# Optimization experiments

Hardware: AMD Instinct MI355X
Metric: run time of the kernel (lower is better)

## Reference

```python
import jax, jax.numpy as jnp
import numpy as np

B, T, LD, PD, W, NL = 2048, 256, 32, 8, 64, 3
TH, CH = LD * 2, W * 2  # token/channel mixing hidden dims (expansion=2)


def setup_inputs() -> dict:
    key = jax.random.key(0)
    ks = jax.random.split(key, 12)
    n = lambda k, s, sc=0.02: jax.random.normal(k, s, jnp.float32) * sc
    return {
        "phys": jax.random.normal(ks[0], (B, T, PD), jnp.float32),
        "latents": jax.random.uniform(ks[1], (B, LD), jnp.float32),
        "pos_emb": n(ks[2], (1, LD, W)),
        "tokW": n(ks[3], (1, W)), "tokb": jnp.zeros((W,), jnp.float32),
        "physW1": n(ks[4], (PD, W)), "physb1": jnp.zeros((W,), jnp.float32),
        "physW2": n(ks[5], (W, W)), "physb2": jnp.zeros((W,), jnp.float32),
        "tn_g": jnp.ones((NL, W), jnp.float32), "tn_b": jnp.zeros((NL, W), jnp.float32),
        "tiW": n(ks[6], (NL, LD, TH)), "tib": jnp.zeros((NL, TH), jnp.float32),
        "toW": n(ks[7], (NL, TH, LD)), "tob": jnp.zeros((NL, LD), jnp.float32),
        "cn_g": jnp.ones((NL, W), jnp.float32), "cn_b": jnp.zeros((NL, W), jnp.float32),
        "ciW": n(ks[8], (NL, W, CH)), "cib": jnp.zeros((NL, CH), jnp.float32),
        "coW": n(ks[9], (NL, CH, W)), "cob": jnp.zeros((NL, W), jnp.float32),
        "hn_g": jnp.ones((W,), jnp.float32), "hn_b": jnp.zeros((W,), jnp.float32),
        "headW": n(ks[10], (W, 1), 0.0002),  # 0.02 init * 0.01 scaling from torch
        "headb": jnp.zeros((1,), jnp.float32),
    }


def _ln(x, g, b):
    m = jnp.mean(x, -1, keepdims=True)
    v = jnp.mean((x - m) ** 2, -1, keepdims=True)
    return (x - m) * jax.lax.rsqrt(v + 1e-5) * g + b


def reference(phys, latents, pos_emb, tokW, tokb, physW1, physb1, physW2, physb2,
              tn_g, tn_b, tiW, tib, toW, tob, cn_g, cn_b, ciW, cib, coW, cob,
              hn_g, hn_b, headW, headb):
    gelu = lambda x: jax.nn.gelu(x, approximate=False)  # torch nn.GELU default (exact)

    def step(current, phys_t):
        # token_projection of current[..., None]: Linear(1, W)
        tokens = current[:, :, None] * tokW[0] + tokb  # [B, LD, W]
        p = gelu(phys_t @ physW1 + physb1) @ physW2 + physb2  # [B, W]
        tokens = tokens + p[:, None, :] + pos_emb
        for i in range(NL):
            # token mixing: LN over width, mix across latent tokens
            mt = jnp.swapaxes(_ln(tokens, tn_g[i], tn_b[i]), 1, 2)  # [B, W, LD]
            mt = gelu(mt @ tiW[i] + tib[i]) @ toW[i] + tob[i]       # [B, W, LD]
            tokens = tokens + jnp.swapaxes(mt, 1, 2)
            # channel mixing over width
            mc = _ln(tokens, cn_g[i], cn_b[i])
            tokens = tokens + (gelu(mc @ ciW[i] + cib[i]) @ coW[i] + cob[i])
        delta = (_ln(tokens, hn_g, hn_b) @ headW + headb)[..., 0]  # [B, LD]
        new = jnp.clip(current + delta, 0.0, 1.0)
        return new, new

    _, outs = jax.lax.scan(step, latents, jnp.swapaxes(phys, 0, 1))  # [T, B, LD]
    return jnp.swapaxes(outs, 0, 1)  # [B, T, LD]
```

## Files before the change

### kernel.cpp

```cpp
#include <hip/hip_runtime.h>
#include <math.h>


namespace {
constexpr int Tt = 256, NL = 3;

typedef float    f32x4 __attribute__((ext_vector_type(4)));
typedef _Float16 half2 __attribute__((ext_vector_type(2)));
typedef _Float16 h16x4 __attribute__((ext_vector_type(4)));
typedef _Float16 h16x8 __attribute__((ext_vector_type(8)));

#define MFMA16(a, b, c) __builtin_amdgcn_mfma_f32_16x16x32_f16((a), (b), (c), 0, 0, 0)

__device__ __forceinline__ half2 h2c(float v) { return (half2)((_Float16)v); }
__device__ __forceinline__ half2 pkrtz(float a, float b) {
    return __builtin_bit_cast(half2, __builtin_amdgcn_cvt_pkrtz(a, b));
}
__device__ __forceinline__ void st4h(short* p, half2 a, half2 b) {
    uint2 v;
    v.x = __builtin_bit_cast(unsigned int, a);
    v.y = __builtin_bit_cast(unsigned int, b);
    *(uint2*)p = v;
}
__device__ __forceinline__ half2 gelu_pk(half2 x) {
    half2 tc = __builtin_elementwise_min(__builtin_elementwise_max(x, h2c(-3.0f)), h2c(3.0f));
    half2 s = (tc * tc) * h2c(0.125f);
    half2 p = s * h2c(0.1455169f) + h2c(-0.446340f);
    p = s * p + h2c(0.604927f);
    p = s * p + h2c(-0.529702f);
    p = s * p + h2c(0.3989423f);
    return x * (h2c(0.5f) + tc * p);
}
__device__ __forceinline__ float gelu_f(float x) {
    float tc = fminf(fmaxf(x, -3.f), 3.f);
    float s = tc * tc;
    float p = fmaf(s, 3.55266e-5f, -8.71758e-4f);
    p = fmaf(s, p, 9.45198e-3f);
    p = fmaf(s, p, -6.62128e-2f);
    p = fmaf(s, p, 0.3989423f);
    return x * fmaf(tc, p, 0.5f);
}
__device__ __forceinline__ float rowsum16(float x) {
    x += __builtin_bit_cast(float, __builtin_amdgcn_update_dpp(0, __builtin_bit_cast(int, x), 0x121, 0xf, 0xf, false));
    x += __builtin_bit_cast(float, __builtin_amdgcn_update_dpp(0, __builtin_bit_cast(int, x), 0x122, 0xf, 0xf, false));
    x += __builtin_bit_cast(float, __builtin_amdgcn_update_dpp(0, __builtin_bit_cast(int, x), 0x124, 0xf, 0xf, false));
    x += __builtin_bit_cast(float, __builtin_amdgcn_update_dpp(0, __builtin_bit_cast(int, x), 0x128, 0xf, 0xf, false));
    return x;
}

__device__ __forceinline__ short f2h(float x) {
    return __builtin_bit_cast(short, (_Float16)x);
}

__global__ void lno_prep(const float* __restrict__ tiW, const float* __restrict__ toW,
                         const float* __restrict__ ciW, const float* __restrict__ coW,
                         const float* __restrict__ physW2, short* __restrict__ wsf) {
    int id = blockIdx.x * 256 + threadIdx.x;
    if (id < 6144) {
        int j = id & 7, lane = (id >> 3) & 63, g = id >> 9;
        int il = g >> 2, u = g & 3;
        int m = u * 16 + (lane & 15), k = (lane >> 4) * 8 + j;
        wsf[id] = f2h(tiW[il * 2048 + k * 64 + m]);
    } else if (id < 12288) {
        int t = id - 6144;
        int j = t & 7, lane = (t >> 3) & 63, g = t >> 9;
        int il = g >> 2, mt2 = (g >> 1) & 1, ks = g & 1;
        int m = mt2 * 16 + (lane & 15), k = ks * 32 + (lane >> 4) * 8 + j;
        wsf[id] = f2h(toW[il * 2048 + k * 32 + m]);
    } else if (id < 36864) {
        int t = id - 12288;
        int j = t & 7, lane = (t >> 3) & 63, g = t >> 9;
        int il = g >> 4, mtc = (g >> 1) & 7, ks = g & 1;
        int m = mtc * 16 + (lane & 15), k = ks * 32 + (lane >> 4) * 8 + j;
        wsf[id] = f2h(ciW[il * 8192 + k * 128 + m]);
    } else if (id < 61440) {
        int t = id - 36864;
        int j = t & 7, lane = (t >> 3) & 63, g = t >> 9;
        int il = g >> 4, nt = (g >> 2) & 3, ks = g & 3;
        int n = nt * 16 + (lane & 15), k = ks * 32 + (lane >> 4) * 8 + j;
        wsf[id] = f2h(coW[il * 8192 + k * 64 + n]);
    } else if (id < 65536) {
        int t = id - 61440;
        int w = t >> 6, k = t & 63;
        ((float*)(wsf + 61440))[t] = physW2[k * 64 + w];
    }
}

__global__ void lno_phys(const float* __restrict__ phys, const float* __restrict__ physW1,
                         const float* __restrict__ physb1, const float* __restrict__ physW2,
                         const float* __restrict__ physb2, short* __restrict__ pout) {
    __shared__ float hsh[4][64];
    const int lane = threadIdx.x & 63, wv = threadIdx.x >> 6;
    const size_t bt = (size_t)blockIdx.x * 4 + wv;
    const float* pt = phys + bt * 8;
    float4 px0 = *(const float4*)pt, px1 = *(const float4*)(pt + 4);
    float a = physb1[lane];
    a = fmaf(px0.x, physW1[0 * 64 + lane], a);
    a = fmaf(px0.y, physW1[1 * 64 + lane], a);
    a = fmaf(px0.z, physW1[2 * 64 + lane], a);
    a = fmaf(px0.w, physW1[3 * 64 + lane], a);
    a = fmaf(px1.x, physW1[4 * 64 + lane], a);
    a = fmaf(px1.y, physW1[5 * 64 + lane], a);
    a = fmaf(px1.z, physW1[6 * 64 + lane], a);
    a = fmaf(px1.w, physW1[7 * 64 + lane], a);
    hsh[wv][lane] = gelu_f(a);
    float acc = physb2[lane];
#pragma unroll
    for (int k = 0; k < 64; ++k) acc = fmaf(hsh[wv][k], physW2[k * 64 + lane], acc);
    pout[bt * 64 + (lane & 15) * 4 + (lane >> 4)] = f2h(acc);
}

__global__ __launch_bounds__(128, 4) void lno_scan(
    const float* __restrict__ latents, const float* __restrict__ pos_emb,
    const float* __restrict__ tokW,    const float* __restrict__ tokb,
    const float* __restrict__ tn_g,    const float* __restrict__ tn_b,
    const float* __restrict__ tib,     const float* __restrict__ tob,
    const float* __restrict__ cn_g,    const float* __restrict__ cn_b,
    const float* __restrict__ cib,     const float* __restrict__ cob,
    const float* __restrict__ hn_g,    const float* __restrict__ hn_b,
    const float* __restrict__ headW,   const float* __restrict__ headb,
    const short* __restrict__ wsf,     const short* pbuf, float* out)
{
    __shared__ __align__(16) short yB[2048];
    __shared__ __align__(16) short hB[4096];
    __shared__ __align__(16) short scr[2][1024];

    const short* tiWF = wsf;
    const short* toWF = wsf + 6144;
    const short* ciWF = wsf + 12288;
    const short* coWF = wsf + 36864;

    const int tid = threadIdx.x, lane = tid & 63, sb = tid >> 6;
    const int q = lane >> 4, c = lane & 15;
    const int b = blockIdx.x;
    short* sc = scr[sb];

    float tokw_r[4], tokb_r[4], gh_r[4];
#pragma unroll
    for (int nt = 0; nt < 4; ++nt) {
        tokw_r[nt] = tokW[nt * 16 + c];
        tokb_r[nt] = tokb[nt * 16 + c];
        gh_r[nt]   = hn_g[nt * 16 + c] * headW[nt * 16 + c];
    }
    float bhp = 0.f;
#pragma unroll
    for (int nt = 0; nt < 4; ++nt) bhp = fmaf(hn_b[nt * 16 + c], headW[nt * 16 + c], bhp);
    const float bh = rowsum16(bhp) + headb[0];

    float pe_r[4][4];
#pragma unroll
    for (int nt = 0; nt < 4; ++nt)
#pragma unroll
        for (int r = 0; r < 4; ++r)
            pe_r[nt][r] = pos_emb[(sb * 16 + q * 4 + r) * 64 + nt * 16 + c];

    f32x4 cur = *(const f32x4*)(latents + b * 32 + sb * 16 + q * 4);
    f32x4 tok[4];

    auto stats = [&](f32x4& mean, f32x4& rsig) {
#pragma unroll
        for (int r = 0; r < 4; ++r) {
            float s = (tok[0][r] + tok[1][r]) + (tok[2][r] + tok[3][r]);
            float qq = tok[0][r] * tok[0][r];
            qq = fmaf(tok[1][r], tok[1][r], qq);
            qq = fmaf(tok[2][r], tok[2][r], qq);
            qq = fmaf(tok[3][r], tok[3][r], qq);
            s = rowsum16(s); qq = rowsum16(qq);
            float m = s * 0.015625f;
            float v = fmaf(-m, m, qq * 0.015625f);
            mean[r] = m;
            rsig[r] = __builtin_amdgcn_rsqf(v + 1e-5f);
        }
    };

#pragma unroll 1
    for (int t = 0; t < Tt; ++t) {
        const h16x4 pv = *(const h16x4*)(pbuf + ((size_t)b * Tt + t) * 64 + c * 4);
#pragma unroll
        for (int nt = 0; nt < 4; ++nt) {
            const float basep = tokb_r[nt] + (float)pv[nt];
#pragma unroll
            for (int r = 0; r < 4; ++r)
                tok[nt][r] = fmaf(cur[r], tokw_r[nt], basep + pe_r[nt][r]);
        }

#pragma unroll 1
        for (int il = 0; il < NL; ++il) {
            f32x4 mean, rsig;
            stats(mean, rsig);
#pragma unroll
            for (int nt = 0; nt < 4; ++nt) {
                const float tng = tn_g[il * 64 + nt * 16 + c];
                const float tnb = tn_b[il * 64 + nt * 16 + c];
                float y0 = fmaf((tok[nt][0] - mean[0]) * rsig[0], tng, tnb);
                float y1 = fmaf((tok[nt][1] - mean[1]) * rsig[1], tng, tnb);
                float y2 = fmaf((tok[nt][2] - mean[2]) * rsig[2], tng, tnb);
                float y3 = fmaf((tok[nt][3] - mean[3]) * rsig[3], tng, tnb);
                st4h(&yB[(nt * 64 + (sb * 2 + (q >> 1)) * 16 + c) * 8 + (q & 1) * 4],
                     pkrtz(y0, y1), pkrtz(y2, y3));
            }
            __syncthreads();
            h16x8 yfrag[4];
#pragma unroll
            for (int nt = 0; nt < 4; ++nt) yfrag[nt] = *(const h16x8*)&yB[(nt * 64 + lane) * 8];

#pragma unroll
            for (int uu = 0; uu < 2; ++uu) {
                const int u = sb * 2 + uu;
                const h16x8 a1 = *(const h16x8*)(tiWF + ((il * 4 + u) * 64 + lane) * 8);
                const f32x4 bi = *(const f32x4*)(tib + il * 64 + u * 16 + q * 4);
#pragma unroll
                for (int nt = 0; nt < 4; ++nt) {
                    f32x4 acc = MFMA16(a1, yfrag[nt], bi);
                    st4h(&hB[sb * 2048 + (nt * 64 + (uu * 2 + (q >> 1)) * 16 + c) * 8 + (q & 1) * 4],
                         gelu_pk(pkrtz(acc[0], acc[1])), gelu_pk(pkrtz(acc[2], acc[3])));
                }
            }
            {
                const f32x4 tb = *(const f32x4*)(tob + il * 32 + sb * 16 + q * 4);
#pragma unroll
                for (int nt = 0; nt < 4; ++nt) tok[nt] += tb;
            }
            __syncthreads();
#pragma unroll
            for (int h = 0; h < 2; ++h) {
                const h16x8 a2 = *(const h16x8*)(toWF + ((il * 4 + sb * 2 + h) * 64 + lane) * 8);
                h16x8 hf[4];
#pragma unroll
                for (int nt = 0; nt < 4; ++nt)
                    hf[nt] = *(const h16x8*)&hB[h * 2048 + (nt * 64 + lane) * 8];
#pragma unroll
                for (int nt = 0; nt < 4; ++nt) tok[nt] = MFMA16(a2, hf[nt], tok[nt]);
            }

            stats(mean, rsig);
#pragma unroll
            for (int nt = 0; nt < 4; ++nt) {
                const float cng = cn_g[il * 64 + nt * 16 + c];
                const float cnb = cn_b[il * 64 + nt * 16 + c];
#pragma unroll
                for (int r = 0; r < 4; ++r) {
                    float v = fmaf((tok[nt][r] - mean[r]) * rsig[r], cng, cnb);
                    sc[(nt >> 1) * 512 + (q * 2 + (c >> 3) + 16 * r + 8 * (nt & 1)) * 8 + (c & 7)] = f2h(v);
                }
            }
            h16x8 b3[2];
            {
                const int lp = ((c >> 2) * 2 + (q & 1)) + 8 * ((c & 3) * 2 + (q >> 1));
#pragma unroll
                for (int ks = 0; ks < 2; ++ks) b3[ks] = *(const h16x8*)&sc[ks * 512 + lp * 8];
            }
#pragma unroll
            for (int nt = 0; nt < 4; ++nt) {
                const float cv = cob[il * 64 + nt * 16 + c];
                tok[nt] += cv;
            }
#pragma unroll
            for (int hh = 0; hh < 2; ++hh) {
#pragma unroll
                for (int mm = 0; mm < 4; ++mm) {
                    const int mtc = hh * 4 + mm;
                    const h16x8 a30 = *(const h16x8*)(ciWF + il * 8192 + (mtc * 2 + 0) * 512 + lane * 8);
                    const h16x8 a31 = *(const h16x8*)(ciWF + il * 8192 + (mtc * 2 + 1) * 512 + lane * 8);
                    const f32x4 bi3 = *(const f32x4*)(cib + il * 128 + mtc * 16 + q * 4);
                    f32x4 acc = MFMA16(a30, b3[0], bi3);
                    acc = MFMA16(a31, b3[1], acc);
                    st4h(&sc[(((mtc >> 1) & 1) * 64 + ((mtc & 1) * 2 + (q >> 1)) * 16 + c) * 8 + (q & 1) * 4],
                         gelu_pk(pkrtz(acc[0], acc[1])), gelu_pk(pkrtz(acc[2], acc[3])));
                }
                h16x8 a4[2];
#pragma unroll
                for (int kk = 0; kk < 2; ++kk) a4[kk] = *(const h16x8*)&sc[(kk * 64 + lane) * 8];
#pragma unroll
                for (int nt = 0; nt < 4; ++nt) {
                    const h16x8 b40 = *(const h16x8*)(coWF + il * 8192 + (nt * 4 + hh * 2 + 0) * 512 + lane * 8);
                    const h16x8 b41 = *(const h16x8*)(coWF + il * 8192 + (nt * 4 + hh * 2 + 1) * 512 + lane * 8);
                    tok[nt] = MFMA16(a4[0], b40, tok[nt]);
                    tok[nt] = MFMA16(a4[1], b41, tok[nt]);
                }
            }
        }

        {
            f32x4 mean, rsig;
            stats(mean, rsig);
#pragma unroll
            for (int r = 0; r < 4; ++r) {
                float l = (tok[0][r] - mean[r]) * gh_r[0];
                l = fmaf(tok[1][r] - mean[r], gh_r[1], l);
                l = fmaf(tok[2][r] - mean[r], gh_r[2], l);
                l = fmaf(tok[3][r] - mean[r], gh_r[3], l);
                l = rowsum16(l);
                float nv = cur[r] + fmaf(rsig[r], l, bh);
                cur[r] = fminf(fmaxf(nv, 0.f), 1.f);
            }
            if (c == 0)
                *(f32x4*)(out + ((size_t)b * Tt + t) * 32 + sb * 16 + q * 4) = cur;
        }
    }
}
}

extern "C" void kernel_launch(void* const* d_in, const int* in_sizes, int n_in,
                              void* d_out, int out_size, void* d_ws, size_t ws_size,
                              hipStream_t stream) {
    (void)in_sizes; (void)n_in; (void)ws_size; (void)out_size;
    const float* phys    = (const float*)d_in[0];
    const float* latents = (const float*)d_in[1];
    const float* pos_emb = (const float*)d_in[2];
    const float* tokW    = (const float*)d_in[3];
    const float* tokb    = (const float*)d_in[4];
    const float* physW1  = (const float*)d_in[5];
    const float* physb1  = (const float*)d_in[6];
    const float* physW2  = (const float*)d_in[7];
    const float* physb2  = (const float*)d_in[8];
    const float* tn_g    = (const float*)d_in[9];
    const float* tn_b    = (const float*)d_in[10];
    const float* tiW     = (const float*)d_in[11];
    const float* tib     = (const float*)d_in[12];
    const float* toW     = (const float*)d_in[13];
    const float* tob     = (const float*)d_in[14];
    const float* cn_g    = (const float*)d_in[15];
    const float* cn_b    = (const float*)d_in[16];
    const float* ciW     = (const float*)d_in[17];
    const float* cib     = (const float*)d_in[18];
    const float* coW     = (const float*)d_in[19];
    const float* cob     = (const float*)d_in[20];
    const float* hn_g    = (const float*)d_in[21];
    const float* hn_b    = (const float*)d_in[22];
    const float* headW   = (const float*)d_in[23];
    const float* headb   = (const float*)d_in[24];

    lno_prep<<<dim3(256), dim3(256), 0, stream>>>(tiW, toW, ciW, coW, physW2, (short*)d_ws);
    lno_phys<<<dim3(131072), dim3(256), 0, stream>>>(phys, physW1, physb1, physW2, physb2,
                                                     (short*)d_out);
    lno_scan<<<dim3(2048), dim3(128), 0, stream>>>(
        latents, pos_emb, tokW, tokb, tn_g, tn_b, tib, tob,
        cn_g, cn_b, cib, cob, hn_g, hn_b, headW, headb,
        (const short*)d_ws, (const short*)d_out, (float*)d_out);
}
```

Baseline: 7.556 ms.

## Pack eight batch rows per block with LDS-resident weights and flag-based wave pairing

The scan kernel now runs 8 batch elements per 1024-thread block, with each pair of waves handling one element. All mixing weights and biases are staged once per block into LDS through global_load_lds, so they are no longer read from global memory on every step. The two __syncthreads per layer are replaced by per-pair release/acquire flag spin-waits, and the token-mixing GEMMs use 16x16x16 MFMA with fragments kept in registers to cut LDS round trips. The phys projection is also prefetched one step ahead. In exchange, the kernel uses about 140KB of LDS, which likely limits it to one block per CU and may reduce the latency hiding it had before.

```diff
diff --git a/kernel.cpp b/kernel.cpp
--- a/kernel.cpp
+++ b/kernel.cpp
@@ -10,9 +10,13 @@
 typedef _Float16 h16x4 __attribute__((ext_vector_type(4)));
 typedef _Float16 h16x8 __attribute__((ext_vector_type(8)));
 
-#define MFMA16(a, b, c) __builtin_amdgcn_mfma_f32_16x16x32_f16((a), (b), (c), 0, 0, 0)
+#define MFMA32(a, b, c) __builtin_amdgcn_mfma_f32_16x16x32_f16((a), (b), (c), 0, 0, 0)
+#define MFMA16(a, b, c) __builtin_amdgcn_mfma_f32_16x16x16f16((a), (b), (c), 0, 0, 0)
+#define REL(p, v) __hip_atomic_store((p), (v), __ATOMIC_RELEASE, __HIP_MEMORY_SCOPE_WORKGROUP)
+#define ACQ(p) __hip_atomic_load((p), __ATOMIC_ACQUIRE, __HIP_MEMORY_SCOPE_WORKGROUP)
 
 __device__ __forceinline__ half2 h2c(float v) { return (half2)((_Float16)v); }
+__device__ __forceinline__ f32x4 f4s(float v) { return (f32x4)v; }
 __device__ __forceinline__ half2 pkrtz(float a, float b) {
     return __builtin_bit_cast(half2, __builtin_amdgcn_cvt_pkrtz(a, b));
 }
@@ -22,6 +26,11 @@
     v.y = __builtin_bit_cast(unsigned int, b);
     *(uint2*)p = v;
 }
+__device__ __forceinline__ h16x4 h4(half2 a, half2 b) {
+    h16x4 v; v[0] = a[0]; v[1] = a[1]; v[2] = b[0]; v[3] = b[1]; return v;
+}
+__device__ __forceinline__ half2 lo2(h16x4 v) { half2 r; r[0] = v[0]; r[1] = v[1]; return r; }
+__device__ __forceinline__ half2 hi2(h16x4 v) { half2 r; r[0] = v[2]; r[1] = v[3]; return r; }
 __device__ __forceinline__ half2 gelu_pk(half2 x) {
     half2 tc = __builtin_elementwise_min(__builtin_elementwise_max(x, h2c(-3.0f)), h2c(3.0f));
     half2 s = (tc * tc) * h2c(0.125f);
@@ -47,7 +56,6 @@
     x += __builtin_bit_cast(float, __builtin_amdgcn_update_dpp(0, __builtin_bit_cast(int, x), 0x128, 0xf, 0xf, false));
     return x;
 }
-
 __device__ __forceinline__ short f2h(float x) {
     return __builtin_bit_cast(short, (_Float16)x);
 }
@@ -57,16 +65,18 @@
                          const float* __restrict__ physW2, short* __restrict__ wsf) {
     int id = blockIdx.x * 256 + threadIdx.x;
     if (id < 6144) {
-        int j = id & 7, lane = (id >> 3) & 63, g = id >> 9;
-        int il = g >> 2, u = g & 3;
-        int m = u * 16 + (lane & 15), k = (lane >> 4) * 8 + j;
-        wsf[id] = f2h(tiW[il * 2048 + k * 64 + m]);
+        int e = id & 255, tile = id >> 8;
+        int lane = e >> 2, j = e & 3;
+        int q = lane >> 4, cc = lane & 15;
+        int kc = tile & 1, u = (tile >> 1) & 3, il = tile >> 3;
+        wsf[id] = f2h(tiW[il * 2048 + (16 * kc + 4 * q + j) * 64 + 16 * u + cc]);
     } else if (id < 12288) {
         int t = id - 6144;
-        int j = t & 7, lane = (t >> 3) & 63, g = t >> 9;
-        int il = g >> 2, mt2 = (g >> 1) & 1, ks = g & 1;
-        int m = mt2 * 16 + (lane & 15), k = ks * 32 + (lane >> 4) * 8 + j;
-        wsf[id] = f2h(toW[il * 2048 + k * 32 + m]);
+        int e = t & 255, tile = t >> 8;
+        int lane = e >> 2, j = e & 3;
+        int q = lane >> 4, cc = lane & 15;
+        int kc = tile & 3, sb = (tile >> 2) & 1, il = tile >> 3;
+        wsf[id] = f2h(toW[il * 2048 + (16 * kc + 4 * q + j) * 32 + 16 * sb + cc]);
     } else if (id < 36864) {
         int t = id - 12288;
         int j = t & 7, lane = (t >> 3) & 63, g = t >> 9;
@@ -110,7 +120,7 @@
     pout[bt * 64 + (lane & 15) * 4 + (lane >> 4)] = f2h(acc);
 }
 
-__global__ __launch_bounds__(128, 4) void lno_scan(
+__global__ __launch_bounds__(1024, 4) void lno_scan(
     const float* __restrict__ latents, const float* __restrict__ pos_emb,
     const float* __restrict__ tokW,    const float* __restrict__ tokb,
     const float* __restrict__ tn_g,    const float* __restrict__ tn_b,
@@ -121,19 +131,44 @@
     const float* __restrict__ headW,   const float* __restrict__ headb,
     const short* __restrict__ wsf,     const short* pbuf, float* out)
 {
-    __shared__ __align__(16) short yB[2048];
-    __shared__ __align__(16) short hB[4096];
-    __shared__ __align__(16) short scr[2][1024];
-
-    const short* tiWF = wsf;
-    const short* toWF = wsf + 6144;
-    const short* ciWF = wsf + 12288;
-    const short* coWF = wsf + 36864;
-
-    const int tid = threadIdx.x, lane = tid & 63, sb = tid >> 6;
+    __shared__ __align__(16) short wAll[61440];
+    __shared__ __align__(16) short tbuf[8][2048];
+    __shared__ __align__(16) float biasL[1632];
+    __shared__ int flags[8][8];
+
+    const int tid = threadIdx.x, lane = tid & 63, wv = tid >> 6;
+    const int sb = wv & 1, tm = wv >> 1, pn = sb ^ 1;
     const int q = lane >> 4, c = lane & 15;
-    const int b = blockIdx.x;
-    short* sc = scr[sb];
+    const int b = blockIdx.x * 8 + tm;
+    short* buf = tbuf[tm];
+    short* mysc = buf + sb * 1024;
+    int* F = flags[tm];
+
+    const short* A1L = wAll;
+    const short* A2L = wAll + 6144;
+    const short* A3L = wAll + 12288;
+    const short* B4L = wAll + 36864;
+
+    if (wv < 15) {
+        const unsigned int* src = (const unsigned int*)wsf;
+#pragma unroll
+        for (int i = 0; i < 8; ++i) {
+            const int cid = wv * 8 + i;
+            __builtin_amdgcn_global_load_lds(src + cid * 256 + lane * 4,
+                                             (unsigned int*)&wAll[cid * 512], 16, 0, 0);
+        }
+    }
+    for (int i = tid; i < 192; i += 1024) {
+        biasL[i] = tib[i];
+        biasL[672 + i]  = tn_g[i];
+        biasL[864 + i]  = tn_b[i];
+        biasL[1056 + i] = cn_g[i];
+        biasL[1248 + i] = cn_b[i];
+        biasL[1440 + i] = cob[i];
+    }
+    for (int i = tid; i < 96;  i += 1024) biasL[192 + i] = tob[i];
+    for (int i = tid; i < 384; i += 1024) biasL[288 + i] = cib[i];
+    if (tid < 64) ((int*)flags)[tid] = 0;
 
     float tokw_r[4], tokb_r[4], gh_r[4];
 #pragma unroll
@@ -147,136 +182,192 @@
     for (int nt = 0; nt < 4; ++nt) bhp = fmaf(hn_b[nt * 16 + c], headW[nt * 16 + c], bhp);
     const float bh = rowsum16(bhp) + headb[0];
 
-    float pe_r[4][4];
+    f32x4 pe4[4];
 #pragma unroll
     for (int nt = 0; nt < 4; ++nt)
 #pragma unroll
         for (int r = 0; r < 4; ++r)
-            pe_r[nt][r] = pos_emb[(sb * 16 + q * 4 + r) * 64 + nt * 16 + c];
+            pe4[nt][r] = pos_emb[(sb * 16 + q * 4 + r) * 64 + nt * 16 + c];
 
     f32x4 cur = *(const f32x4*)(latents + b * 32 + sb * 16 + q * 4);
     f32x4 tok[4];
 
+    __syncthreads();
+
     auto stats = [&](f32x4& mean, f32x4& rsig) {
+        f32x4 s4 = (tok[0] + tok[1]) + (tok[2] + tok[3]);
+        f32x4 q4 = tok[0] * tok[0];
+        q4 = __builtin_elementwise_fma(tok[1], tok[1], q4);
+        q4 = __builtin_elementwise_fma(tok[2], tok[2], q4);
+        q4 = __builtin_elementwise_fma(tok[3], tok[3], q4);
 #pragma unroll
         for (int r = 0; r < 4; ++r) {
-            float s = (tok[0][r] + tok[1][r]) + (tok[2][r] + tok[3][r]);
-            float qq = tok[0][r] * tok[0][r];
-            qq = fmaf(tok[1][r], tok[1][r], qq);
-            qq = fmaf(tok[2][r], tok[2][r], qq);
-            qq = fmaf(tok[3][r], tok[3][r], qq);
-            s = rowsum16(s); qq = rowsum16(qq);
-            float m = s * 0.015625f;
+            float ss = rowsum16(s4[r]);
+            float qq = rowsum16(q4[r]);
+            float m = ss * 0.015625f;
             float v = fmaf(-m, m, qq * 0.015625f);
             mean[r] = m;
             rsig[r] = __builtin_amdgcn_rsqf(v + 1e-5f);
         }
     };
 
+    const short* pb = pbuf + (size_t)b * Tt * 64 + c * 4;
+    h16x4 pvc = *(const h16x4*)pb;
+
 #pragma unroll 1
     for (int t = 0; t < Tt; ++t) {
-        const h16x4 pv = *(const h16x4*)(pbuf + ((size_t)b * Tt + t) * 64 + c * 4);
+        const h16x4 pv = pvc;
+        if (t + 1 < Tt) pvc = *(const h16x4*)(pb + (t + 1) * 64);
+
 #pragma unroll
         for (int nt = 0; nt < 4; ++nt) {
-            const float basep = tokb_r[nt] + (float)pv[nt];
-#pragma unroll
-            for (int r = 0; r < 4; ++r)
-                tok[nt][r] = fmaf(cur[r], tokw_r[nt], basep + pe_r[nt][r]);
+            const f32x4 bp = f4s(tokb_r[nt] + (float)pv[nt]);
+            tok[nt] = __builtin_elementwise_fma(cur, f4s(tokw_r[nt]), pe4[nt] + bp);
         }
 
 #pragma unroll 1
         for (int il = 0; il < NL; ++il) {
+            const int g = t * 3 + il + 1;
             f32x4 mean, rsig;
             stats(mean, rsig);
+            h16x4 b1own[4];
 #pragma unroll
             for (int nt = 0; nt < 4; ++nt) {
-                const float tng = tn_g[il * 64 + nt * 16 + c];
-                const float tnb = tn_b[il * 64 + nt * 16 + c];
-                float y0 = fmaf((tok[nt][0] - mean[0]) * rsig[0], tng, tnb);
-                float y1 = fmaf((tok[nt][1] - mean[1]) * rsig[1], tng, tnb);
-                float y2 = fmaf((tok[nt][2] - mean[2]) * rsig[2], tng, tnb);
-                float y3 = fmaf((tok[nt][3] - mean[3]) * rsig[3], tng, tnb);
-                st4h(&yB[(nt * 64 + (sb * 2 + (q >> 1)) * 16 + c) * 8 + (q & 1) * 4],
-                     pkrtz(y0, y1), pkrtz(y2, y3));
-            }
-            __syncthreads();
-            h16x8 yfrag[4];
-#pragma unroll
-            for (int nt = 0; nt < 4; ++nt) yfrag[nt] = *(const h16x8*)&yB[(nt * 64 + lane) * 8];
-
+                const float tng = biasL[672 + il * 64 + nt * 16 + c];
+                const float tnb = biasL[864 + il * 64 + nt * 16 + c];
+                f32x4 y = __builtin_elementwise_fma((tok[nt] - mean) * rsig,
+                                                    f4s(tng), f4s(tnb));
+                half2 d0 = pkrtz(y[0], y[1]), d1 = pkrtz(y[2], y[3]);
+                b1own[nt] = h4(d0, d1);
+                st4h(&buf[sb * 1024 + (nt * 64 + lane) * 4], d0, d1);
+            }
+            if (lane == 0) REL(&F[sb], g);
+            {
+                const f32x4 tb = *(const f32x4*)&biasL[192 + il * 32 + sb * 16 + q * 4];
+#pragma unroll
+                for (int nt = 0; nt < 4; ++nt) tok[nt] += tb;
+            }
+            f32x4 hacc[2][4];
 #pragma unroll
             for (int uu = 0; uu < 2; ++uu) {
-                const int u = sb * 2 + uu;
-                const h16x8 a1 = *(const h16x8*)(tiWF + ((il * 4 + u) * 64 + lane) * 8);
-                const f32x4 bi = *(const f32x4*)(tib + il * 64 + u * 16 + q * 4);
+                const int u = 2 * sb + uu;
+                const h16x4 a1 = *(const h16x4*)(A1L + (((il * 4 + u) * 2) + sb) * 256 + lane * 4);
+                const f32x4 bi = *(const f32x4*)&biasL[il * 64 + u * 16 + q * 4];
+#pragma unroll
+                for (int nt = 0; nt < 4; ++nt) hacc[uu][nt] = MFMA16(a1, b1own[nt], bi);
+            }
+            while (ACQ(&F[pn]) < g) {}
+            h16x4 b1p[4];
+#pragma unroll
+            for (int nt = 0; nt < 4; ++nt)
+                b1p[nt] = *(const h16x4*)&buf[pn * 1024 + (nt * 64 + lane) * 4];
+#pragma unroll
+            for (int uu = 0; uu < 2; ++uu) {
+                const int u = 2 * sb + uu;
+                const h16x4 a1 = *(const h16x4*)(A1L + (((il * 4 + u) * 2) + pn) * 256 + lane * 4);
+#pragma unroll
+                for (int nt = 0; nt < 4; ++nt) hacc[uu][nt] = MFMA16(a1, b1p[nt], hacc[uu][nt]);
+            }
+            if (sb == 1 && lane == 0) REL(&F[5], g);
+            h16x4 b2own[2][4];
+#pragma unroll
+            for (int uu = 0; uu < 2; ++uu)
 #pragma unroll
                 for (int nt = 0; nt < 4; ++nt) {
-                    f32x4 acc = MFMA16(a1, yfrag[nt], bi);
-                    st4h(&hB[sb * 2048 + (nt * 64 + (uu * 2 + (q >> 1)) * 16 + c) * 8 + (q & 1) * 4],
-                         gelu_pk(pkrtz(acc[0], acc[1])), gelu_pk(pkrtz(acc[2], acc[3])));
-                }
-            }
-            {
-                const f32x4 tb = *(const f32x4*)(tob + il * 32 + sb * 16 + q * 4);
-#pragma unroll
-                for (int nt = 0; nt < 4; ++nt) tok[nt] += tb;
-            }
-            __syncthreads();
-#pragma unroll
-            for (int h = 0; h < 2; ++h) {
-                const h16x8 a2 = *(const h16x8*)(toWF + ((il * 4 + sb * 2 + h) * 64 + lane) * 8);
-                h16x8 hf[4];
-#pragma unroll
-                for (int nt = 0; nt < 4; ++nt)
-                    hf[nt] = *(const h16x8*)&hB[h * 2048 + (nt * 64 + lane) * 8];
-#pragma unroll
-                for (int nt = 0; nt < 4; ++nt) tok[nt] = MFMA16(a2, hf[nt], tok[nt]);
+                    half2 e0 = gelu_pk(pkrtz(hacc[uu][nt][0], hacc[uu][nt][1]));
+                    half2 e1 = gelu_pk(pkrtz(hacc[uu][nt][2], hacc[uu][nt][3]));
+                    b2own[uu][nt] = h4(e0, e1);
+                }
+            if (sb == 0) {
+                while (ACQ(&F[5]) < g) {}
+#pragma unroll
+                for (int uu = 0; uu < 2; ++uu)
+#pragma unroll
+                    for (int nt = 0; nt < 4; ++nt)
+                        st4h(&buf[((uu * 4 + nt) * 64 + lane) * 4], lo2(b2own[uu][nt]), hi2(b2own[uu][nt]));
+                if (lane == 0) REL(&F[2], g);
+#pragma unroll
+                for (int kc = 0; kc < 2; ++kc) {
+                    const h16x4 a2 = *(const h16x4*)(A2L + ((il * 2 + sb) * 4 + kc) * 256 + lane * 4);
+#pragma unroll
+                    for (int nt = 0; nt < 4; ++nt) tok[nt] = MFMA16(a2, b2own[kc][nt], tok[nt]);
+                }
+                while (ACQ(&F[3]) < g) {}
+#pragma unroll
+                for (int kc = 2; kc < 4; ++kc) {
+                    const h16x4 a2 = *(const h16x4*)(A2L + ((il * 2 + sb) * 4 + kc) * 256 + lane * 4);
+#pragma unroll
+                    for (int nt = 0; nt < 4; ++nt) {
+                        const h16x4 b2p = *(const h16x4*)&buf[(((kc - 2) * 4 + nt) * 64 + lane) * 4];
+                        tok[nt] = MFMA16(a2, b2p, tok[nt]);
+                    }
+                }
+                if (lane == 0) REL(&F[4], g);
+            } else {
+#pragma unroll
+                for (int kcl = 0; kcl < 2; ++kcl) {
+                    const int kc = 2 + kcl;
+                    const h16x4 a2 = *(const h16x4*)(A2L + ((il * 2 + sb) * 4 + kc) * 256 + lane * 4);
+#pragma unroll
+                    for (int nt = 0; nt < 4; ++nt) tok[nt] = MFMA16(a2, b2own[kcl][nt], tok[nt]);
+                }
+                while (ACQ(&F[2]) < g) {}
+#pragma unroll
+                for (int kc = 0; kc < 2; ++kc) {
+                    const h16x4 a2 = *(const h16x4*)(A2L + ((il * 2 + sb) * 4 + kc) * 256 + lane * 4);
+#pragma unroll
+                    for (int nt = 0; nt < 4; ++nt) {
+                        const h16x4 b2p = *(const h16x4*)&buf[((kc * 4 + nt) * 64 + lane) * 4];
+                        tok[nt] = MFMA16(a2, b2p, tok[nt]);
+                    }
+                }
+#pragma unroll
+                for (int uu = 0; uu < 2; ++uu)
+#pragma unroll
+                    for (int nt = 0; nt < 4; ++nt)
+                        st4h(&buf[((uu * 4 + nt) * 64 + lane) * 4], lo2(b2own[uu][nt]), hi2(b2own[uu][nt]));
+                if (lane == 0) REL(&F[3], g);
             }
 
             stats(mean, rsig);
+            if (sb == 1) { while (ACQ(&F[4]) < g) {} }
 #pragma unroll
             for (int nt = 0; nt < 4; ++nt) {
-                const float cng = cn_g[il * 64 + nt * 16 + c];
-                const float cnb = cn_b[il * 64 + nt * 16 + c];
+                const float cng = biasL[1056 + il * 64 + nt * 16 + c];
+                const float cnb = biasL[1248 + il * 64 + nt * 16 + c];
 #pragma unroll
                 for (int r = 0; r < 4; ++r) {
                     float v = fmaf((tok[nt][r] - mean[r]) * rsig[r], cng, cnb);
-                    sc[(nt >> 1) * 512 + (q * 2 + (c >> 3) + 16 * r + 8 * (nt & 1)) * 8 + (c & 7)] = f2h(v);
+                    mysc[((nt >> 1) * 64 + (2 * (nt & 1) + (c >> 3)) * 16 + 4 * q + r) * 8 + (c & 7)] = f2h(v);
                 }
             }
             h16x8 b3[2];
-            {
-                const int lp = ((c >> 2) * 2 + (q & 1)) + 8 * ((c & 3) * 2 + (q >> 1));
-#pragma unroll
-                for (int ks = 0; ks < 2; ++ks) b3[ks] = *(const h16x8*)&sc[ks * 512 + lp * 8];
-            }
-#pragma unroll
-            for (int nt = 0; nt < 4; ++nt) {
-                const float cv = cob[il * 64 + nt * 16 + c];
-                tok[nt] += cv;
-            }
+#pragma unroll
+            for (int kc = 0; kc < 2; ++kc) b3[kc] = *(const h16x8*)&mysc[(kc * 64 + lane) * 8];
+#pragma unroll
+            for (int nt = 0; nt < 4; ++nt) tok[nt] += f4s(biasL[1440 + il * 64 + nt * 16 + c]);
 #pragma unroll
             for (int hh = 0; hh < 2; ++hh) {
 #pragma unroll
                 for (int mm = 0; mm < 4; ++mm) {
                     const int mtc = hh * 4 + mm;
-                    const h16x8 a30 = *(const h16x8*)(ciWF + il * 8192 + (mtc * 2 + 0) * 512 + lane * 8);
-                    const h16x8 a31 = *(const h16x8*)(ciWF + il * 8192 + (mtc * 2 + 1) * 512 + lane * 8);
-                    const f32x4 bi3 = *(const f32x4*)(cib + il * 128 + mtc * 16 + q * 4);
-                    f32x4 acc = MFMA16(a30, b3[0], bi3);
-                    acc = MFMA16(a31, b3[1], acc);
-                    st4h(&sc[(((mtc >> 1) & 1) * 64 + ((mtc & 1) * 2 + (q >> 1)) * 16 + c) * 8 + (q & 1) * 4],
+                    const h16x8 a30 = *(const h16x8*)(A3L + il * 8192 + (mtc * 2 + 0) * 512 + lane * 8);
+                    const h16x8 a31 = *(const h16x8*)(A3L + il * 8192 + (mtc * 2 + 1) * 512 + lane * 8);
+                    const f32x4 bi3 = *(const f32x4*)&biasL[288 + il * 128 + mtc * 16 + q * 4];
+                    f32x4 acc = MFMA32(a30, b3[0], bi3);
+                    acc = MFMA32(a31, b3[1], acc);
+                    st4h(&mysc[(((mtc >> 1) & 1) * 64 + ((mtc & 1) * 2 + (q >> 1)) * 16 + c) * 8 + (q & 1) * 4],
                          gelu_pk(pkrtz(acc[0], acc[1])), gelu_pk(pkrtz(acc[2], acc[3])));
                 }
                 h16x8 a4[2];
 #pragma unroll
-                for (int kk = 0; kk < 2; ++kk) a4[kk] = *(const h16x8*)&sc[(kk * 64 + lane) * 8];
+                for (int kf = 0; kf < 2; ++kf) a4[kf] = *(const h16x8*)&mysc[(kf * 64 + lane) * 8];
 #pragma unroll
                 for (int nt = 0; nt < 4; ++nt) {
-                    const h16x8 b40 = *(const h16x8*)(coWF + il * 8192 + (nt * 4 + hh * 2 + 0) * 512 + lane * 8);
-                    const h16x8 b41 = *(const h16x8*)(coWF + il * 8192 + (nt * 4 + hh * 2 + 1) * 512 + lane * 8);
-                    tok[nt] = MFMA16(a4[0], b40, tok[nt]);
-                    tok[nt] = MFMA16(a4[1], b41, tok[nt]);
+                    const h16x8 b40 = *(const h16x8*)(B4L + il * 8192 + (nt * 4 + hh * 2 + 0) * 512 + lane * 8);
+                    const h16x8 b41 = *(const h16x8*)(B4L + il * 8192 + (nt * 4 + hh * 2 + 1) * 512 + lane * 8);
+                    tok[nt] = MFMA32(a4[0], b40, tok[nt]);
+                    tok[nt] = MFMA32(a4[1], b41, tok[nt]);
                 }
             }
         }
@@ -284,16 +375,16 @@
         {
             f32x4 mean, rsig;
             stats(mean, rsig);
-#pragma unroll
-            for (int r = 0; r < 4; ++r) {
-                float l = (tok[0][r] - mean[r]) * gh_r[0];
-                l = fmaf(tok[1][r] - mean[r], gh_r[1], l);
-                l = fmaf(tok[2][r] - mean[r], gh_r[2], l);
-                l = fmaf(tok[3][r] - mean[r], gh_r[3], l);
-                l = rowsum16(l);
-                float nv = cur[r] + fmaf(rsig[r], l, bh);
-                cur[r] = fminf(fmaxf(nv, 0.f), 1.f);
-            }
+            f32x4 l4 = (tok[0] - mean) * f4s(gh_r[0]);
+            l4 = __builtin_elementwise_fma(tok[1] - mean, f4s(gh_r[1]), l4);
+            l4 = __builtin_elementwise_fma(tok[2] - mean, f4s(gh_r[2]), l4);
+            l4 = __builtin_elementwise_fma(tok[3] - mean, f4s(gh_r[3]), l4);
+            f32x4 ls;
+#pragma unroll
+            for (int r = 0; r < 4; ++r) ls[r] = rowsum16(l4[r]);
+            f32x4 nv = cur + __builtin_elementwise_fma(rsig, ls, f4s(bh));
+            nv = __builtin_elementwise_min(__builtin_elementwise_max(nv, f4s(0.f)), f4s(1.f));
+            cur = nv;
             if (c == 0)
                 *(f32x4*)(out + ((size_t)b * Tt + t) * 32 + sb * 16 + q * 4) = cur;
         }
@@ -334,7 +425,7 @@
     lno_prep<<<dim3(256), dim3(256), 0, stream>>>(tiW, toW, ciW, coW, physW2, (short*)d_ws);
     lno_phys<<<dim3(131072), dim3(256), 0, stream>>>(phys, physW1, physb1, physW2, physb2,
                                                      (short*)d_out);
-    lno_scan<<<dim3(2048), dim3(128), 0, stream>>>(
+    lno_scan<<<dim3(256), dim3(1024), 0, stream>>>(
         latents, pos_emb, tokW, tokb, tn_g, tn_b, tib, tob,
         cn_g, cn_b, cib, cob, hn_g, hn_b, headW, headb,
         (const short*)d_ws, (const short*)d_out, (float*)d_out);
```

New measurement: 7.246 ms. -4.1%, faster.
